# Performance work log

Measured on AMD Instinct MI355X. Metric: run time of the kernel, lower is better.

## Reference

```python
import jax, jax.numpy as jnp
import numpy as np

N = 50000       # nodes
E = 800000      # edges (avg degree 16)
F_IN = 128      # in_feats
H = 128         # h_feats
C = 16          # num_classes
EPS = 1e-5      # BatchNorm eps


def setup_inputs() -> dict:
    key = jax.random.key(0)
    ks = jax.random.split(key, 26)
    rn = lambda k, shape: jax.random.normal(k, shape, dtype=jnp.float32) * 0.05
    zeros = lambda d: jnp.zeros((d,), jnp.float32)
    ones = lambda d: jnp.ones((d,), jnp.float32)
    return {
        "features": jax.random.normal(ks[0], (N, F_IN), dtype=jnp.float32),
        "src": jax.random.randint(ks[1], (E,), 0, N),
        "dst": jax.random.randint(ks[2], (E,), 0, N),
        # input_encoder
        "W_in": rn(ks[3], (F_IN, H)), "b_in": zeros(H),
        # SAGEConv layer 0: H -> 2H (fc_self, fc_neigh, bias)
        "Ws0": rn(ks[4], (H, 2 * H)), "Wn0": rn(ks[5], (H, 2 * H)), "bs0": zeros(2 * H),
        # BatchNorm1d(2H) eval-mode stats
        "g0": ones(2 * H), "bt0": zeros(2 * H),
        "m0": rn(ks[6], (2 * H,)),
        "v0": jax.random.uniform(ks[7], (2 * H,), jnp.float32, 0.5, 1.5),
        # SAGEConv layer 1: 2H -> H
        "Ws1": rn(ks[8], (2 * H, H)), "Wn1": rn(ks[9], (2 * H, H)), "bs1": zeros(H),
        # BatchNorm1d(H)
        "g1": ones(H), "bt1": zeros(H),
        "m1": rn(ks[10], (H,)),
        "v1": jax.random.uniform(ks[11], (H,), jnp.float32, 0.5, 1.5),
        # relation_encoder: 2H -> H
        "Wr": rn(ks[12], (2 * H, H)), "br": zeros(H),
        # classifier: H -> H//2 -> C
        "Wc1": rn(ks[13], (H, H // 2)), "bc1": zeros(H // 2),
        "Wc2": rn(ks[14], (H // 2, C)), "bc2": zeros(C),
    }


def _bn(x, g, b, m, v):
    # eval-mode BatchNorm1d with running stats
    return (x - m) * jax.lax.rsqrt(v + EPS) * g + b


def _sage(h, src, dst, Ws, Wn, b, inv_deg):
    # DGL SAGEConv 'mean': out = fc_self(h_dst) + fc_neigh(mean_{u in N(v)} h_u) + bias
    neigh = jax.ops.segment_sum(h[src], dst, num_segments=N) * inv_deg  # [N, d_in]
    return h @ Ws + neigh @ Wn + b


def reference(features, src, dst, W_in, b_in, Ws0, Wn0, bs0, g0, bt0, m0, v0,
              Ws1, Wn1, bs1, g1, bt1, m1, v1, Wr, br, Wc1, bc1, Wc2, bc2):
    deg = jax.ops.segment_sum(jnp.ones((E,), jnp.float32), dst, num_segments=N)
    inv_deg = (1.0 / jnp.maximum(deg, 1.0))[:, None]  # [N, 1]

    h0 = jax.nn.relu(features @ W_in + b_in)                       # [N, H]
    h = jax.nn.relu(_bn(_sage(h0, src, dst, Ws0, Wn0, bs0, inv_deg), g0, bt0, m0, v0))  # [N, 2H]
    h = jax.nn.relu(_bn(_sage(h, src, dst, Ws1, Wn1, bs1, inv_deg), g1, bt1, m1, v1))   # [N, H]

    h_final = jax.nn.relu(jnp.concatenate([h0, h], axis=1) @ Wr + br)  # [N, H]
    return jax.nn.relu(h_final @ Wc1 + bc1) @ Wc2 + bc2                # [N, C]
```

## Files before the change

kernel.cpp:

```cpp
#include <hip/hip_runtime.h>

typedef short v8s __attribute__((ext_vector_type(8)));
typedef float v4f __attribute__((ext_vector_type(4)));
typedef unsigned short u16;
typedef unsigned int u32;

#define NNODES 50000
#define NEDGES 800000
#define CSTRIDE 64

#define NB 512
#define BSPAN 98
#define BCAP 2048
#define EBLK 98
#define NBU 511

__device__ __forceinline__ float bf2f(u16 b) {
    u32 u = ((u32)b) << 16;
    return __builtin_bit_cast(float, u);
}
__device__ __forceinline__ u16 f2bf(float f) {
    u32 u = __builtin_bit_cast(u32, f);
    u32 r = (u + 0x7fffu + ((u >> 16) & 1u)) >> 16;
    return (u16)r;
}

struct PackDesc { const float* B1; const float* B2; int K1, K2, N, csplit, start; u16* out; };
struct PackArgs { PackDesc d[6]; int total; };

__global__ __launch_bounds__(256) void pack_all(PackArgs pa) {
    int tid = blockIdx.x * 256 + threadIdx.x;
    if (tid >= pa.total) return;
    int s = 0;
    for (int i = 1; i < 6; i++)
        if (tid >= pa.d[i].start) s = i;
    const PackDesc& D = pa.d[s];
    int t = tid - D.start;
    int frag = t >> 9;
    int rem = t & 511;
    int lane = rem >> 3;
    int j = rem & 7;
    int nf = D.N >> 4;
    int kt = frag / nf, nt = frag - kt * nf;
    int k = kt * 32 + (lane >> 4) * 8 + j;
    int n = nt * 16 + (lane & 15);
    float v;
    if (D.csplit)
        v = (n < D.csplit) ? D.B1[(size_t)k * D.csplit + n]
                           : D.B2[(size_t)k * (D.N - D.csplit) + (n - D.csplit)];
    else
        v = (k < D.K1) ? D.B1[(size_t)k * D.N + n]
                       : D.B2[(size_t)(k - D.K1) * D.N + n];
    D.out[t] = f2bf(v);
}

__global__ __launch_bounds__(256) void prep_epi(
    const float* b_in, const float* bs0, const float* g0, const float* bt0,
    const float* m0, const float* v0,
    const float* bs1, const float* g1, const float* bt1, const float* m1, const float* v1,
    const float* br, const float* bc1, const float* bc2,
    float* sc_in, float* sh_in, float* sc0, float* sh0, float* sc1, float* sh1,
    float* sc_r, float* sh_r, float* sh_c1, float* sh_c2) {
    int t = threadIdx.x;
    if (t < 128) { sc_in[t] = 1.f; sh_in[t] = b_in[t]; }
    if (t < 256) {
        float s = g0[t] * rsqrtf(v0[t] + 1e-5f);
        sc0[t] = s;
        sh0[t] = (bs0[t] - m0[t]) * s + bt0[t];
    }
    if (t < 128) {
        float s = g1[t] * rsqrtf(v1[t] + 1e-5f);
        sc1[t] = s;
        sh1[t] = (bs1[t] - m1[t]) * s + bt1[t];
    }
    if (t < 128) { sc_r[t] = 1.f; sh_r[t] = br[t]; }
    if (t < 64)  { sh_c1[t] = bc1[t]; }
    if (t < 16)  { sh_c2[t] = bc2[t]; }
}

template <int BN, int CW, int KT, int KSPLIT, bool RELU, bool F32OUT, bool AF32>
__device__ __forceinline__ void gemm_body(
    int bx,
    const void* __restrict__ A0v, int lda0,
    const void* __restrict__ A1v, int lda1,
    int M,
    const v8s* __restrict__ Bp,
    const float* __restrict__ scale, const float* __restrict__ shift,
    u16* __restrict__ C, float* __restrict__ Cf, int ldc) {
    constexpr int NFW = BN / 16 / CW;
    constexpr int RW = 4 / CW;
    int lane = threadIdx.x & 63;
    int wave = threadIdx.x >> 6;
    int colw = wave % CW;
    int roww = wave / CW;
    int quad = lane >> 4;
    int l16 = lane & 15;
    int base = bx * (64 * RW) + roww * 64;

    v4f acc[4][NFW];
#pragma unroll
    for (int rg = 0; rg < 4; rg++)
#pragma unroll
        for (int nt = 0; nt < NFW; nt++) acc[rg][nt] = (v4f)0.0f;

    size_t o0[4], o1[4];
#pragma unroll
    for (int rg = 0; rg < 4; rg++) {
        int r = base + rg * 16 + l16;
        if (r > M - 1) r = M - 1;
        o0[rg] = (size_t)r * lda0 + quad * 8;
        o1[rg] = (size_t)r * lda1 + quad * 8;
    }

    auto load_a = [&](const void* Av, size_t off) -> v8s {
        if constexpr (AF32) {
            const float* p = (const float*)Av + off;
            float4 x = *(const float4*)p;
            float4 y = *(const float4*)(p + 4);
            v8s a;
            a[0] = (short)f2bf(x.x); a[1] = (short)f2bf(x.y);
            a[2] = (short)f2bf(x.z); a[3] = (short)f2bf(x.w);
            a[4] = (short)f2bf(y.x); a[5] = (short)f2bf(y.y);
            a[6] = (short)f2bf(y.z); a[7] = (short)f2bf(y.w);
            return a;
        } else {
            return *(const v8s*)((const u16*)Av + off);
        }
    };

#pragma unroll
    for (int kt = 0; kt < KT; kt++) {
        v8s a[4];
#pragma unroll
        for (int rg = 0; rg < 4; rg++) {
            if (kt < KSPLIT) a[rg] = load_a(A0v, o0[rg] + kt * 32);
            else             a[rg] = load_a(A1v, o1[rg] + (size_t)(kt - KSPLIT) * 32);
        }
        const v8s* bb = Bp + (size_t)kt * (BN / 16) * 64 + (colw * NFW) * 64 + lane;
#pragma unroll
        for (int nt = 0; nt < NFW; nt++) {
            v8s b = bb[nt * 64];
#pragma unroll
            for (int rg = 0; rg < 4; rg++)
                acc[rg][nt] = __builtin_amdgcn_mfma_f32_16x16x32_bf16(a[rg], b, acc[rg][nt], 0, 0, 0);
        }
    }

    int colbase = colw * (NFW * 16);
#pragma unroll
    for (int rg = 0; rg < 4; rg++) {
        int rbase = base + rg * 16 + quad * 4;
#pragma unroll
        for (int nt = 0; nt < NFW; nt++) {
            int col = colbase + nt * 16 + l16;
            float s = scale[col], sh = shift[col];
#pragma unroll
            for (int i = 0; i < 4; i++) {
                int row = rbase + i;
                if (row < M) {
                    float v = acc[rg][nt][i] * s + sh;
                    if (RELU) v = v > 0.f ? v : 0.f;
                    if (F32OUT) Cf[(size_t)row * ldc + col] = v;
                    else C[(size_t)row * ldc + col] = f2bf(v);
                }
            }
        }
    }
}

__global__ __launch_bounds__(256) void mega_binA_h0(
    const int* __restrict__ src, const int* __restrict__ dst,
    int* __restrict__ gcur, u32* __restrict__ gbuf,
    const float* __restrict__ features,
    const v8s* __restrict__ Winp,
    const float* __restrict__ sc_in, const float* __restrict__ sh_in,
    u16* __restrict__ hcat0) {
    int bx = blockIdx.x;
    if (bx < EBLK) {
        __shared__ int hist[NB];
        __shared__ int lbase[NB];
        int t = threadIdx.x;
        for (int i = t; i < NB; i += 256) hist[i] = 0;
        __syncthreads();
        int ebase = bx * 8192;
#pragma unroll
        for (int c = 0; c < 8; c++) {
            int e0 = ebase + c * 1024 + t * 4;
            if (e0 + 4 <= NEDGES) {
                int4 d4 = *(const int4*)(dst + e0);
                atomicAdd(&hist[d4.x / BSPAN], 1);
                atomicAdd(&hist[d4.y / BSPAN], 1);
                atomicAdd(&hist[d4.z / BSPAN], 1);
                atomicAdd(&hist[d4.w / BSPAN], 1);
            } else {
#pragma unroll
                for (int j = 0; j < 4; j++) {
                    int e = e0 + j;
                    if (e < NEDGES) atomicAdd(&hist[dst[e] / BSPAN], 1);
                }
            }
        }
        __syncthreads();
        for (int i = t; i < NB; i += 256) {
            int c = hist[i];
            lbase[i] = c ? atomicAdd(&gcur[i], c) : 0;
            hist[i] = 0;
        }
        __syncthreads();
#pragma unroll
        for (int c = 0; c < 8; c++) {
            int e0 = ebase + c * 1024 + t * 4;
            if (e0 + 4 <= NEDGES) {
                int4 s4 = *(const int4*)(src + e0);
                int4 d4 = *(const int4*)(dst + e0);
                int ss[4] = {s4.x, s4.y, s4.z, s4.w};
                int dd[4] = {d4.x, d4.y, d4.z, d4.w};
#pragma unroll
                for (int j = 0; j < 4; j++) {
                    int b = dd[j] / BSPAN;
                    int dl = dd[j] - b * BSPAN;
                    int p = atomicAdd(&hist[b], 1);
                    int idx = lbase[b] + p;
                    if (idx < BCAP)
                        gbuf[(size_t)b * BCAP + idx] = ((u32)dl << 16) | (u32)ss[j];
                }
            } else {
#pragma unroll
                for (int j = 0; j < 4; j++) {
                    int e = e0 + j;
                    if (e < NEDGES) {
                        int d = dst[e];
                        int b = d / BSPAN;
                        int dl = d - b * BSPAN;
                        int p = atomicAdd(&hist[b], 1);
                        int idx = lbase[b] + p;
                        if (idx < BCAP)
                            gbuf[(size_t)b * BCAP + idx] = ((u32)dl << 16) | (u32)src[e];
                    }
                }
            }
        }
    } else {
        gemm_body<128, 4, 4, 4, true, false, true>(
            bx - EBLK, features, 128, features, 128, NNODES,
            Winp, sc_in, sh_in, hcat0, nullptr, 256);
    }
}

__global__ __launch_bounds__(1024) void fill_bg(
    const u32* __restrict__ gbuf, const int* __restrict__ gcur,
    u16* __restrict__ csr, int* __restrict__ cursor,
    const u16* __restrict__ H, u16* __restrict__ D) {
    __shared__ u16 lcsr[BSPAN * CSTRIDE];
    __shared__ int lcur[BSPAN];
    int b = blockIdx.x;
    int t = threadIdx.x;
    int v0 = b * BSPAN;
    int span = NNODES - v0;
    if (span > BSPAN) span = BSPAN;
    for (int i = t; i < BSPAN; i += 1024) lcur[i] = 0;
    __syncthreads();
    int cnt = gcur[b];
    if (cnt > BCAP) cnt = BCAP;
    for (int i = t; i < cnt; i += 1024) {
        u32 pk = gbuf[(size_t)b * BCAP + i];
        int dl = pk >> 16;
        int p = atomicAdd(&lcur[dl], 1);
        if (p < CSTRIDE) lcsr[(dl << 6) + p] = (u16)(pk & 0xffffu);
    }
    __syncthreads();
    {
        const u32* lw = (const u32*)lcsr;
        u32* gw = (u32*)(csr + ((size_t)v0 << 6));
        int nw = span * (CSTRIDE / 2);
        for (int i = t; i < nw; i += 1024) gw[i] = lw[i];
        for (int i = t; i < span; i += 1024) cursor[v0 + i] = lcur[i];
    }
    int lane = t & 63;
    int wv = t >> 6;
    for (int i = wv; i < span; i += 16) {
        int d = lcur[i];
        if (d > CSTRIDE) d = CSTRIDE;
        float s = 1.0f / (float)(d > 0 ? d : 1);
        const u16* Hl = H + lane * 2;
        const u16* nl = &lcsr[i << 6];
        float a0 = 0.f, a1 = 0.f, b0 = 0.f, b1 = 0.f;
        float c0 = 0.f, c1 = 0.f, d0 = 0.f, d1 = 0.f;
        int e = 0;
        for (; e + 4 <= d; e += 4) {
            int u0 = nl[e], u1 = nl[e + 1], u2 = nl[e + 2], u3 = nl[e + 3];
            u32 w0 = *(const u32*)(Hl + (size_t)u0 * 256);
            u32 w1 = *(const u32*)(Hl + (size_t)u1 * 256);
            u32 w2 = *(const u32*)(Hl + (size_t)u2 * 256);
            u32 w3 = *(const u32*)(Hl + (size_t)u3 * 256);
            a0 += bf2f((u16)w0); a1 += bf2f((u16)(w0 >> 16));
            b0 += bf2f((u16)w1); b1 += bf2f((u16)(w1 >> 16));
            c0 += bf2f((u16)w2); c1 += bf2f((u16)(w2 >> 16));
            d0 += bf2f((u16)w3); d1 += bf2f((u16)(w3 >> 16));
        }
        for (; e < d; e++) {
            int u = nl[e];
            u32 w = *(const u32*)(Hl + (size_t)u * 256);
            a0 += bf2f((u16)w); a1 += bf2f((u16)(w >> 16));
        }
        a0 = (a0 + b0) + (c0 + d0);
        a1 = (a1 + b1) + (c1 + d1);
        u32 o = (u32)f2bf(a0 * s) | ((u32)f2bf(a1 * s) << 16);
        *(u32*)(D + (size_t)(v0 + i) * 256 + lane * 2) = o;
    }
}

__global__ __launch_bounds__(256) void gemm_h1ps(
    const u16* __restrict__ A,
    const v8s* __restrict__ B0,
    const float* __restrict__ sc0, const float* __restrict__ sh0,
    const v8s* __restrict__ B1,
    u16* __restrict__ ps, int M) {
    constexpr int LSTR = 264;
    __shared__ u16 h1s[64 * LSTR];
    int lane = threadIdx.x & 63;
    int wave = threadIdx.x >> 6;
    int quad = lane >> 4;
    int l16 = lane & 15;
    int base = blockIdx.x * 64;

    v4f acc[4][4];
#pragma unroll
    for (int rg = 0; rg < 4; rg++)
#pragma unroll
        for (int nt = 0; nt < 4; nt++) acc[rg][nt] = (v4f)0.0f;

    size_t o0[4];
#pragma unroll
    for (int rg = 0; rg < 4; rg++) {
        int r = base + rg * 16 + l16;
        if (r > M - 1) r = M - 1;
        o0[rg] = (size_t)r * 256 + quad * 8;
    }

#pragma unroll
    for (int kt = 0; kt < 8; kt++) {
        v8s a[4];
#pragma unroll
        for (int rg = 0; rg < 4; rg++) a[rg] = *(const v8s*)(A + o0[rg] + kt * 32);
        const v8s* bb = B0 + (size_t)kt * 16 * 64 + (wave * 4) * 64 + lane;
#pragma unroll
        for (int nt = 0; nt < 4; nt++) {
            v8s b = bb[nt * 64];
#pragma unroll
            for (int rg = 0; rg < 4; rg++)
                acc[rg][nt] = __builtin_amdgcn_mfma_f32_16x16x32_bf16(a[rg], b, acc[rg][nt], 0, 0, 0);
        }
    }
    int colbase = wave * 64;
#pragma unroll
    for (int rg = 0; rg < 4; rg++) {
        int rowL = rg * 16 + quad * 4;
#pragma unroll
        for (int nt = 0; nt < 4; nt++) {
            int col = colbase + nt * 16 + l16;
            float s = sc0[col], sh = sh0[col];
#pragma unroll
            for (int i = 0; i < 4; i++) {
                float v = acc[rg][nt][i] * s + sh;
                v = v > 0.f ? v : 0.f;
                h1s[(rowL + i) * LSTR + col] = f2bf(v);
            }
        }
    }
    __syncthreads();

#pragma unroll
    for (int rg = 0; rg < 4; rg++)
#pragma unroll
        for (int nt = 0; nt < 4; nt++) acc[rg][nt] = (v4f)0.0f;
#pragma unroll
    for (int kt = 0; kt < 8; kt++) {
        v8s a[4];
#pragma unroll
        for (int rg = 0; rg < 4; rg++)
            a[rg] = *(const v8s*)(&h1s[(rg * 16 + l16) * LSTR + quad * 8 + kt * 32]);
        const v8s* bb = B1 + (size_t)kt * 16 * 64 + (wave * 4) * 64 + lane;
#pragma unroll
        for (int nt = 0; nt < 4; nt++) {
            v8s b = bb[nt * 64];
#pragma unroll
            for (int rg = 0; rg < 4; rg++)
                acc[rg][nt] = __builtin_amdgcn_mfma_f32_16x16x32_bf16(a[rg], b, acc[rg][nt], 0, 0, 0);
        }
    }
#pragma unroll
    for (int rg = 0; rg < 4; rg++) {
        int rbase = base + rg * 16 + quad * 4;
#pragma unroll
        for (int nt = 0; nt < 4; nt++) {
            int col = colbase + nt * 16 + l16;
#pragma unroll
            for (int i = 0; i < 4; i++) {
                int row = rbase + i;
                if (row < M) ps[(size_t)row * 256 + col] = f2bf(acc[rg][nt][i]);
            }
        }
    }
}

__global__ __launch_bounds__(256) void agg_h2(
    const int* __restrict__ cursor, const u16* __restrict__ csr,
    const u16* __restrict__ ps,
    const float* __restrict__ sc1, const float* __restrict__ sh1,
    u16* __restrict__ h2, int n) {
    int v = blockIdx.x * 4 + (threadIdx.x >> 6);
    if (v >= n) return;
    int lane = threadIdx.x & 63;
    int d = cursor[v];
    if (d > CSTRIDE) d = CSTRIDE;
    int e0 = v << 6;
    int e1 = e0 + d;
    float s = 1.0f / (float)(d > 0 ? d : 1);
    const u16* Pn = ps + 128 + lane * 2;
    float a0 = 0.f, a1 = 0.f, b0 = 0.f, b1 = 0.f;
    float c0 = 0.f, c1 = 0.f, d0 = 0.f, d1 = 0.f;
    int e = e0;
    for (; e + 4 <= e1; e += 4) {
        int u0 = csr[e], u1 = csr[e + 1], u2 = csr[e + 2], u3 = csr[e + 3];
        u32 w0 = *(const u32*)(Pn + (size_t)u0 * 256);
        u32 w1 = *(const u32*)(Pn + (size_t)u1 * 256);
        u32 w2 = *(const u32*)(Pn + (size_t)u2 * 256);
        u32 w3 = *(const u32*)(Pn + (size_t)u3 * 256);
        a0 += bf2f((u16)w0); a1 += bf2f((u16)(w0 >> 16));
        b0 += bf2f((u16)w1); b1 += bf2f((u16)(w1 >> 16));
        c0 += bf2f((u16)w2); c1 += bf2f((u16)(w2 >> 16));
        d0 += bf2f((u16)w3); d1 += bf2f((u16)(w3 >> 16));
    }
    for (; e < e1; e++) {
        int u = csr[e];
        u32 w = *(const u32*)(Pn + (size_t)u * 256);
        a0 += bf2f((u16)w); a1 += bf2f((u16)(w >> 16));
    }
    a0 = (a0 + b0) + (c0 + d0);
    a1 = (a1 + b1) + (c1 + d1);
    u32 wv = *(const u32*)(ps + (size_t)v * 256 + lane * 2);
    int col = lane * 2;
    float x0 = (bf2f((u16)wv) + a0 * s) * sc1[col] + sh1[col];
    float x1 = (bf2f((u16)(wv >> 16)) + a1 * s) * sc1[col + 1] + sh1[col + 1];
    x0 = x0 > 0.f ? x0 : 0.f;
    x1 = x1 > 0.f ? x1 : 0.f;
    u32 o = (u32)f2bf(x0) | ((u32)f2bf(x1) << 16);
    *(u32*)(h2 + (size_t)v * 128 + lane * 2) = o;
}

__global__ __launch_bounds__(256) void gemm_chain(
    const u16* __restrict__ hcat0,
    const u16* __restrict__ h2,
    const v8s* __restrict__ Wrp, const float* __restrict__ sc_r, const float* __restrict__ sh_r,
    const v8s* __restrict__ Wm1p, const float* __restrict__ sh_c1,
    const v8s* __restrict__ Wm2p, const float* __restrict__ sh_c2,
    float* __restrict__ out, int M) {
    constexpr int LS = 136;
    __shared__ u16 tile[64 * LS];
    int lane = threadIdx.x & 63;
    int wv = threadIdx.x >> 6;
    int quad = lane >> 4;
    int l16 = lane & 15;
    int base = blockIdx.x * 64;

    v4f acc[4][2];
#pragma unroll
    for (int rg = 0; rg < 4; rg++)
#pragma unroll
        for (int nt = 0; nt < 2; nt++) acc[rg][nt] = (v4f)0.0f;
    size_t o0[4], o1[4];
#pragma unroll
    for (int rg = 0; rg < 4; rg++) {
        int r = base + rg * 16 + l16;
        if (r > M - 1) r = M - 1;
        o0[rg] = (size_t)r * 256 + quad * 8;
        o1[rg] = (size_t)r * 128 + quad * 8;
    }
#pragma unroll
    for (int kt = 0; kt < 8; kt++) {
        v8s a[4];
#pragma unroll
        for (int rg = 0; rg < 4; rg++) {
            if (kt < 4) a[rg] = *(const v8s*)(hcat0 + o0[rg] + kt * 32);
            else        a[rg] = *(const v8s*)(h2 + o1[rg] + (size_t)(kt - 4) * 32);
        }
        const v8s* bb = Wrp + (size_t)kt * 8 * 64 + (wv * 2) * 64 + lane;
#pragma unroll
        for (int nt = 0; nt < 2; nt++) {
            v8s b = bb[nt * 64];
#pragma unroll
            for (int rg = 0; rg < 4; rg++)
                acc[rg][nt] = __builtin_amdgcn_mfma_f32_16x16x32_bf16(a[rg], b, acc[rg][nt], 0, 0, 0);
        }
    }
    {
        int colbase = wv * 32;
#pragma unroll
        for (int rg = 0; rg < 4; rg++) {
            int rowL = rg * 16 + quad * 4;
#pragma unroll
            for (int nt = 0; nt < 2; nt++) {
                int col = colbase + nt * 16 + l16;
                float s = sc_r[col], sh = sh_r[col];
#pragma unroll
                for (int i = 0; i < 4; i++) {
                    float v = acc[rg][nt][i] * s + sh;
                    v = v > 0.f ? v : 0.f;
                    tile[(rowL + i) * LS + col] = f2bf(v);
                }
            }
        }
    }
    __syncthreads();

    v4f a2[4];
#pragma unroll
    for (int rg = 0; rg < 4; rg++) a2[rg] = (v4f)0.0f;
#pragma unroll
    for (int kt = 0; kt < 4; kt++) {
        v8s a[4];
#pragma unroll
        for (int rg = 0; rg < 4; rg++)
            a[rg] = *(const v8s*)(&tile[(rg * 16 + l16) * LS + quad * 8 + kt * 32]);
        v8s b = Wm1p[(size_t)kt * 4 * 64 + wv * 64 + lane];
#pragma unroll
        for (int rg = 0; rg < 4; rg++)
            a2[rg] = __builtin_amdgcn_mfma_f32_16x16x32_bf16(a[rg], b, a2[rg], 0, 0, 0);
    }
    __syncthreads();
    {
        int col = wv * 16 + l16;
        float sh = sh_c1[col];
#pragma unroll
        for (int rg = 0; rg < 4; rg++) {
            int rowL = rg * 16 + quad * 4;
#pragma unroll
            for (int i = 0; i < 4; i++) {
                float v = a2[rg][i] + sh;
                v = v > 0.f ? v : 0.f;
                tile[(rowL + i) * LS + col] = f2bf(v);
            }
        }
    }
    __syncthreads();

    v4f a3 = (v4f)0.0f;
#pragma unroll
    for (int kt = 0; kt < 2; kt++) {
        v8s a = *(const v8s*)(&tile[(wv * 16 + l16) * LS + quad * 8 + kt * 32]);
        v8s b = Wm2p[kt * 64 + lane];
        a3 = __builtin_amdgcn_mfma_f32_16x16x32_bf16(a, b, a3, 0, 0, 0);
    }
    int row = base + wv * 16 + quad * 4;
    float sh = sh_c2[l16];
#pragma unroll
    for (int i = 0; i < 4; i++) {
        int r = row + i;
        if (r < M) out[(size_t)r * 16 + l16] = a3[i] + sh;
    }
}

extern "C" void kernel_launch(void* const* d_in, const int* in_sizes, int n_in,
                              void* d_out, int out_size, void* d_ws, size_t ws_size,
                              hipStream_t stream) {
    const int N = NNODES;
    const float* features = (const float*)d_in[0];
    const int* src = (const int*)d_in[1];
    const int* dst = (const int*)d_in[2];
    float* out = (float*)d_out;

    char* w = (char*)d_ws;
    auto alloc = [&](size_t bytes) -> char* {
        char* p = w;
        w += (bytes + 255) & ~(size_t)255;
        return p;
    };
    int*   cursor = (int*)alloc((size_t)N * 4);
    u16*   csr    = (u16*)alloc((size_t)N * CSTRIDE * 2);
    u16*   hcat0  = (u16*)alloc((size_t)N * 256 * 2);
    u16*   ps     = (u16*)alloc((size_t)N * 256 * 2);
    u16*   h2     = (u16*)alloc((size_t)N * 128 * 2);
    u32*   gbuf   = (u32*)alloc((size_t)NB * BCAP * 4);
    int*   gcur   = (int*)alloc((size_t)NB * 4);
    u16*   Winp   = (u16*)alloc(128 * 128 * 2);
    u16*   Wc0p   = (u16*)alloc(256 * 256 * 2);
    u16*   Wsn1p  = (u16*)alloc(256 * 256 * 2);
    u16*   Wrp    = (u16*)alloc(256 * 128 * 2);
    u16*   Wm1p   = (u16*)alloc(128 * 64 * 2);
    u16*   Wm2p   = (u16*)alloc(64 * 16 * 2);
    float* sc_in = (float*)alloc(128 * 4); float* sh_in = (float*)alloc(128 * 4);
    float* sc0   = (float*)alloc(256 * 4); float* sh0   = (float*)alloc(256 * 4);
    float* sc1   = (float*)alloc(128 * 4); float* sh1   = (float*)alloc(128 * 4);
    float* sc_r  = (float*)alloc(128 * 4); float* sh_r  = (float*)alloc(128 * 4);
    float* sh_c1 = (float*)alloc(64 * 4);
    float* sh_c2 = (float*)alloc(16 * 4);

    hipMemsetAsync(gcur, 0, (size_t)NB * 4, stream);
    prep_epi<<<1, 256, 0, stream>>>((const float*)d_in[4], (const float*)d_in[7],
                                    (const float*)d_in[8], (const float*)d_in[9],
                                    (const float*)d_in[10], (const float*)d_in[11],
                                    (const float*)d_in[14], (const float*)d_in[15],
                                    (const float*)d_in[16], (const float*)d_in[17],
                                    (const float*)d_in[18], (const float*)d_in[20],
                                    (const float*)d_in[22], (const float*)d_in[24],
                                    sc_in, sh_in, sc0, sh0, sc1, sh1,
                                    sc_r, sh_r, sh_c1, sh_c2);

    PackArgs pa;
    int st = 0;
    auto seg = [&](int i, const float* B1, const float* B2, int K1, int K2,
                   int Nn, int csp, u16* o) {
        pa.d[i] = {B1, B2, K1, K2, Nn, csp, st, o};
        st += (K1 + K2) * Nn;
    };
    seg(0, (const float*)d_in[3], nullptr, 128, 0, 128, 0, Winp);
    seg(1, (const float*)d_in[5], (const float*)d_in[6], 128, 128, 256, 0, Wc0p);
    seg(2, (const float*)d_in[12], (const float*)d_in[13], 256, 0, 256, 128, Wsn1p);
    seg(3, (const float*)d_in[19], nullptr, 256, 0, 128, 0, Wrp);
    seg(4, (const float*)d_in[21], nullptr, 128, 0, 64, 0, Wm1p);
    seg(5, (const float*)d_in[23], nullptr, 64, 0, 16, 0, Wm2p);
    pa.total = st;
    pack_all<<<(st + 255) / 256, 256, 0, stream>>>(pa);

    int gb64 = (N + 63) / 64;
    mega_binA_h0<<<EBLK + gb64, 256, 0, stream>>>(
        src, dst, gcur, gbuf, features, (const v8s*)Winp, sc_in, sh_in, hcat0);
    fill_bg<<<NBU, 1024, 0, stream>>>(gbuf, gcur, csr, cursor, hcat0, hcat0 + 128);
    gemm_h1ps<<<gb64, 256, 0, stream>>>(hcat0, (const v8s*)Wc0p, sc0, sh0,
                                        (const v8s*)Wsn1p, ps, N);
    agg_h2<<<(N + 3) / 4, 256, 0, stream>>>(cursor, csr, ps, sc1, sh1, h2, N);
    gemm_chain<<<gb64, 256, 0, stream>>>(
        hcat0, h2, (const v8s*)Wrp, sc_r, sh_r,
        (const v8s*)Wm1p, sh_c1, (const v8s*)Wm2p, sh_c2, out, N);
}
```

Before: 265.0 us.

## Fuse neighbor-mean gathers into the consuming GEMM kernels via shared memory

The layer-0 neighbor mean moves out of the CSR fill kernel and into the h1/ps GEMM kernel, which gathers each 64-row tile's neighbor means into LDS and feeds them to the MFMA loop. The layer-1 aggregation kernel is folded into the final chain GEMM the same way, so the hcat0 upper half and the h2 intermediate are never written to or re-read from global memory, and one launch disappears. The gather loop is unrolled by 8 for more memory-level parallelism, and h0 now has a compact 128-wide stride. In exchange, GEMM blocks stall on latency-bound gathers before their MFMA work, and the added LDS per block may reduce occupancy.

```diff
diff --git a/kernel.cpp b/kernel.cpp
--- a/kernel.cpp
+++ b/kernel.cpp
@@ -174,7 +174,7 @@
     const float* __restrict__ features,
     const v8s* __restrict__ Winp,
     const float* __restrict__ sc_in, const float* __restrict__ sh_in,
-    u16* __restrict__ hcat0) {
+    u16* __restrict__ h0) {
     int bx = blockIdx.x;
     if (bx < EBLK) {
         __shared__ int hist[NB];
@@ -243,14 +243,13 @@
     } else {
         gemm_body<128, 4, 4, 4, true, false, true>(
             bx - EBLK, features, 128, features, 128, NNODES,
-            Winp, sc_in, sh_in, hcat0, nullptr, 256);
-    }
-}
-
-__global__ __launch_bounds__(1024) void fill_bg(
+            Winp, sc_in, sh_in, h0, nullptr, 128);
+    }
+}
+
+__global__ __launch_bounds__(256) void fill_b(
     const u32* __restrict__ gbuf, const int* __restrict__ gcur,
-    u16* __restrict__ csr, int* __restrict__ cursor,
-    const u16* __restrict__ H, u16* __restrict__ D) {
+    u16* __restrict__ csr, int* __restrict__ cursor) {
     __shared__ u16 lcsr[BSPAN * CSTRIDE];
     __shared__ int lcur[BSPAN];
     int b = blockIdx.x;
@@ -258,65 +257,83 @@
     int v0 = b * BSPAN;
     int span = NNODES - v0;
     if (span > BSPAN) span = BSPAN;
-    for (int i = t; i < BSPAN; i += 1024) lcur[i] = 0;
+    for (int i = t; i < BSPAN; i += 256) lcur[i] = 0;
     __syncthreads();
     int cnt = gcur[b];
     if (cnt > BCAP) cnt = BCAP;
-    for (int i = t; i < cnt; i += 1024) {
+    for (int i = t; i < cnt; i += 256) {
         u32 pk = gbuf[(size_t)b * BCAP + i];
         int dl = pk >> 16;
         int p = atomicAdd(&lcur[dl], 1);
         if (p < CSTRIDE) lcsr[(dl << 6) + p] = (u16)(pk & 0xffffu);
     }
     __syncthreads();
-    {
-        const u32* lw = (const u32*)lcsr;
-        u32* gw = (u32*)(csr + ((size_t)v0 << 6));
-        int nw = span * (CSTRIDE / 2);
-        for (int i = t; i < nw; i += 1024) gw[i] = lw[i];
-        for (int i = t; i < span; i += 1024) cursor[v0 + i] = lcur[i];
-    }
-    int lane = t & 63;
-    int wv = t >> 6;
-    for (int i = wv; i < span; i += 16) {
-        int d = lcur[i];
-        if (d > CSTRIDE) d = CSTRIDE;
-        float s = 1.0f / (float)(d > 0 ? d : 1);
-        const u16* Hl = H + lane * 2;
-        const u16* nl = &lcsr[i << 6];
-        float a0 = 0.f, a1 = 0.f, b0 = 0.f, b1 = 0.f;
-        float c0 = 0.f, c1 = 0.f, d0 = 0.f, d1 = 0.f;
-        int e = 0;
-        for (; e + 4 <= d; e += 4) {
-            int u0 = nl[e], u1 = nl[e + 1], u2 = nl[e + 2], u3 = nl[e + 3];
-            u32 w0 = *(const u32*)(Hl + (size_t)u0 * 256);
-            u32 w1 = *(const u32*)(Hl + (size_t)u1 * 256);
-            u32 w2 = *(const u32*)(Hl + (size_t)u2 * 256);
-            u32 w3 = *(const u32*)(Hl + (size_t)u3 * 256);
-            a0 += bf2f((u16)w0); a1 += bf2f((u16)(w0 >> 16));
-            b0 += bf2f((u16)w1); b1 += bf2f((u16)(w1 >> 16));
-            c0 += bf2f((u16)w2); c1 += bf2f((u16)(w2 >> 16));
-            d0 += bf2f((u16)w3); d1 += bf2f((u16)(w3 >> 16));
-        }
-        for (; e < d; e++) {
-            int u = nl[e];
-            u32 w = *(const u32*)(Hl + (size_t)u * 256);
-            a0 += bf2f((u16)w); a1 += bf2f((u16)(w >> 16));
-        }
-        a0 = (a0 + b0) + (c0 + d0);
-        a1 = (a1 + b1) + (c1 + d1);
-        u32 o = (u32)f2bf(a0 * s) | ((u32)f2bf(a1 * s) << 16);
-        *(u32*)(D + (size_t)(v0 + i) * 256 + lane * 2) = o;
-    }
-}
-
-__global__ __launch_bounds__(256) void gemm_h1ps(
-    const u16* __restrict__ A,
+    const u32* lw = (const u32*)lcsr;
+    u32* gw = (u32*)(csr + ((size_t)v0 << 6));
+    int nw = span * (CSTRIDE / 2);
+    for (int i = t; i < nw; i += 256) gw[i] = lw[i];
+    for (int i = t; i < span; i += 256) cursor[v0 + i] = lcur[i];
+}
+
+__device__ __forceinline__ u32 gather_mean2(
+    const u16* __restrict__ nl, int d, const u16* __restrict__ Hl, int ldh) {
+    float a0 = 0.f, a1 = 0.f, b0 = 0.f, b1 = 0.f;
+    float c0 = 0.f, c1 = 0.f, d0 = 0.f, d1 = 0.f;
+    float e0 = 0.f, e1 = 0.f, f0 = 0.f, f1 = 0.f;
+    float g0 = 0.f, g1 = 0.f, h0_ = 0.f, h1_ = 0.f;
+    int e = 0;
+    for (; e + 8 <= d; e += 8) {
+        int u0 = nl[e], u1 = nl[e + 1], u2 = nl[e + 2], u3 = nl[e + 3];
+        int u4 = nl[e + 4], u5 = nl[e + 5], u6 = nl[e + 6], u7 = nl[e + 7];
+        u32 w0 = *(const u32*)(Hl + (size_t)u0 * ldh);
+        u32 w1 = *(const u32*)(Hl + (size_t)u1 * ldh);
+        u32 w2 = *(const u32*)(Hl + (size_t)u2 * ldh);
+        u32 w3 = *(const u32*)(Hl + (size_t)u3 * ldh);
+        u32 w4 = *(const u32*)(Hl + (size_t)u4 * ldh);
+        u32 w5 = *(const u32*)(Hl + (size_t)u5 * ldh);
+        u32 w6 = *(const u32*)(Hl + (size_t)u6 * ldh);
+        u32 w7 = *(const u32*)(Hl + (size_t)u7 * ldh);
+        a0 += bf2f((u16)w0); a1 += bf2f((u16)(w0 >> 16));
+        b0 += bf2f((u16)w1); b1 += bf2f((u16)(w1 >> 16));
+        c0 += bf2f((u16)w2); c1 += bf2f((u16)(w2 >> 16));
+        d0 += bf2f((u16)w3); d1 += bf2f((u16)(w3 >> 16));
+        e0 += bf2f((u16)w4); e1 += bf2f((u16)(w4 >> 16));
+        f0 += bf2f((u16)w5); f1 += bf2f((u16)(w5 >> 16));
+        g0 += bf2f((u16)w6); g1 += bf2f((u16)(w6 >> 16));
+        h0_ += bf2f((u16)w7); h1_ += bf2f((u16)(w7 >> 16));
+    }
+    for (; e + 4 <= d; e += 4) {
+        int u0 = nl[e], u1 = nl[e + 1], u2 = nl[e + 2], u3 = nl[e + 3];
+        u32 w0 = *(const u32*)(Hl + (size_t)u0 * ldh);
+        u32 w1 = *(const u32*)(Hl + (size_t)u1 * ldh);
+        u32 w2 = *(const u32*)(Hl + (size_t)u2 * ldh);
+        u32 w3 = *(const u32*)(Hl + (size_t)u3 * ldh);
+        a0 += bf2f((u16)w0); a1 += bf2f((u16)(w0 >> 16));
+        b0 += bf2f((u16)w1); b1 += bf2f((u16)(w1 >> 16));
+        c0 += bf2f((u16)w2); c1 += bf2f((u16)(w2 >> 16));
+        d0 += bf2f((u16)w3); d1 += bf2f((u16)(w3 >> 16));
+    }
+    for (; e < d; e++) {
+        int u = nl[e];
+        u32 w = *(const u32*)(Hl + (size_t)u * ldh);
+        a0 += bf2f((u16)w); a1 += bf2f((u16)(w >> 16));
+    }
+    float s = 1.0f / (float)(d > 0 ? d : 1);
+    float r0 = ((a0 + b0) + (c0 + d0)) + ((e0 + f0) + (g0 + h0_));
+    float r1 = ((a1 + b1) + (c1 + d1)) + ((e1 + f1) + (g1 + h1_));
+    return (u32)f2bf(r0 * s) | ((u32)f2bf(r1 * s) << 16);
+}
+
+__global__ __launch_bounds__(256) void h1ps_g(
+    const int* __restrict__ cursor, const u16* __restrict__ csr,
+    const u16* __restrict__ h0,
     const v8s* __restrict__ B0,
     const float* __restrict__ sc0, const float* __restrict__ sh0,
     const v8s* __restrict__ B1,
     u16* __restrict__ ps, int M) {
+    constexpr int NLS = 136;
     constexpr int LSTR = 264;
+    __shared__ u16 n0s[64 * NLS];
     __shared__ u16 h1s[64 * LSTR];
     int lane = threadIdx.x & 63;
     int wave = threadIdx.x >> 6;
@@ -324,6 +341,18 @@
     int l16 = lane & 15;
     int base = blockIdx.x * 64;
 
+    for (int i = wave; i < 64; i += 4) {
+        int v = base + i;
+        u32 o = 0;
+        if (v < M) {
+            int d = cursor[v];
+            if (d > CSTRIDE) d = CSTRIDE;
+            o = gather_mean2(csr + ((size_t)v << 6), d, h0 + lane * 2, 128);
+        }
+        *(u32*)(&n0s[i * NLS + lane * 2]) = o;
+    }
+    __syncthreads();
+
     v4f acc[4][4];
 #pragma unroll
     for (int rg = 0; rg < 4; rg++)
@@ -335,14 +364,17 @@
     for (int rg = 0; rg < 4; rg++) {
         int r = base + rg * 16 + l16;
         if (r > M - 1) r = M - 1;
-        o0[rg] = (size_t)r * 256 + quad * 8;
+        o0[rg] = (size_t)r * 128 + quad * 8;
     }
 
 #pragma unroll
     for (int kt = 0; kt < 8; kt++) {
         v8s a[4];
 #pragma unroll
-        for (int rg = 0; rg < 4; rg++) a[rg] = *(const v8s*)(A + o0[rg] + kt * 32);
+        for (int rg = 0; rg < 4; rg++) {
+            if (kt < 4) a[rg] = *(const v8s*)(h0 + o0[rg] + kt * 32);
+            else        a[rg] = *(const v8s*)(&n0s[(rg * 16 + l16) * NLS + quad * 8 + (kt - 4) * 32]);
+        }
         const v8s* bb = B0 + (size_t)kt * 16 * 64 + (wave * 4) * 64 + lane;
 #pragma unroll
         for (int nt = 0; nt < 4; nt++) {
@@ -404,59 +436,17 @@
     }
 }
 
-__global__ __launch_bounds__(256) void agg_h2(
+__global__ __launch_bounds__(256) void chain_all(
     const int* __restrict__ cursor, const u16* __restrict__ csr,
     const u16* __restrict__ ps,
     const float* __restrict__ sc1, const float* __restrict__ sh1,
-    u16* __restrict__ h2, int n) {
-    int v = blockIdx.x * 4 + (threadIdx.x >> 6);
-    if (v >= n) return;
-    int lane = threadIdx.x & 63;
-    int d = cursor[v];
-    if (d > CSTRIDE) d = CSTRIDE;
-    int e0 = v << 6;
-    int e1 = e0 + d;
-    float s = 1.0f / (float)(d > 0 ? d : 1);
-    const u16* Pn = ps + 128 + lane * 2;
-    float a0 = 0.f, a1 = 0.f, b0 = 0.f, b1 = 0.f;
-    float c0 = 0.f, c1 = 0.f, d0 = 0.f, d1 = 0.f;
-    int e = e0;
-    for (; e + 4 <= e1; e += 4) {
-        int u0 = csr[e], u1 = csr[e + 1], u2 = csr[e + 2], u3 = csr[e + 3];
-        u32 w0 = *(const u32*)(Pn + (size_t)u0 * 256);
-        u32 w1 = *(const u32*)(Pn + (size_t)u1 * 256);
-        u32 w2 = *(const u32*)(Pn + (size_t)u2 * 256);
-        u32 w3 = *(const u32*)(Pn + (size_t)u3 * 256);
-        a0 += bf2f((u16)w0); a1 += bf2f((u16)(w0 >> 16));
-        b0 += bf2f((u16)w1); b1 += bf2f((u16)(w1 >> 16));
-        c0 += bf2f((u16)w2); c1 += bf2f((u16)(w2 >> 16));
-        d0 += bf2f((u16)w3); d1 += bf2f((u16)(w3 >> 16));
-    }
-    for (; e < e1; e++) {
-        int u = csr[e];
-        u32 w = *(const u32*)(Pn + (size_t)u * 256);
-        a0 += bf2f((u16)w); a1 += bf2f((u16)(w >> 16));
-    }
-    a0 = (a0 + b0) + (c0 + d0);
-    a1 = (a1 + b1) + (c1 + d1);
-    u32 wv = *(const u32*)(ps + (size_t)v * 256 + lane * 2);
-    int col = lane * 2;
-    float x0 = (bf2f((u16)wv) + a0 * s) * sc1[col] + sh1[col];
-    float x1 = (bf2f((u16)(wv >> 16)) + a1 * s) * sc1[col + 1] + sh1[col + 1];
-    x0 = x0 > 0.f ? x0 : 0.f;
-    x1 = x1 > 0.f ? x1 : 0.f;
-    u32 o = (u32)f2bf(x0) | ((u32)f2bf(x1) << 16);
-    *(u32*)(h2 + (size_t)v * 128 + lane * 2) = o;
-}
-
-__global__ __launch_bounds__(256) void gemm_chain(
-    const u16* __restrict__ hcat0,
-    const u16* __restrict__ h2,
+    const u16* __restrict__ h0,
     const v8s* __restrict__ Wrp, const float* __restrict__ sc_r, const float* __restrict__ sh_r,
     const v8s* __restrict__ Wm1p, const float* __restrict__ sh_c1,
     const v8s* __restrict__ Wm2p, const float* __restrict__ sh_c2,
     float* __restrict__ out, int M) {
     constexpr int LS = 136;
+    __shared__ u16 h2s[64 * LS];
     __shared__ u16 tile[64 * LS];
     int lane = threadIdx.x & 63;
     int wv = threadIdx.x >> 6;
@@ -464,26 +454,44 @@
     int l16 = lane & 15;
     int base = blockIdx.x * 64;
 
+    for (int i = wv; i < 64; i += 4) {
+        int v = base + i;
+        u32 o = 0;
+        if (v < M) {
+            int d = cursor[v];
+            if (d > CSTRIDE) d = CSTRIDE;
+            u32 nm = gather_mean2(csr + ((size_t)v << 6), d, ps + 128 + lane * 2, 256);
+            u32 sv = *(const u32*)(ps + (size_t)v * 256 + lane * 2);
+            int col = lane * 2;
+            float x0 = (bf2f((u16)sv) + bf2f((u16)nm)) * sc1[col] + sh1[col];
+            float x1 = (bf2f((u16)(sv >> 16)) + bf2f((u16)(nm >> 16))) * sc1[col + 1] + sh1[col + 1];
+            x0 = x0 > 0.f ? x0 : 0.f;
+            x1 = x1 > 0.f ? x1 : 0.f;
+            o = (u32)f2bf(x0) | ((u32)f2bf(x1) << 16);
+        }
+        *(u32*)(&h2s[i * LS + lane * 2]) = o;
+    }
+    __syncthreads();
+
     v4f acc[4][2];
 #pragma unroll
     for (int rg = 0; rg < 4; rg++)
 #pragma unroll
         for (int nt = 0; nt < 2; nt++) acc[rg][nt] = (v4f)0.0f;
-    size_t o0[4], o1[4];
+    size_t o0[4];
 #pragma unroll
     for (int rg = 0; rg < 4; rg++) {
         int r = base + rg * 16 + l16;
         if (r > M - 1) r = M - 1;
-        o0[rg] = (size_t)r * 256 + quad * 8;
-        o1[rg] = (size_t)r * 128 + quad * 8;
+        o0[rg] = (size_t)r * 128 + quad * 8;
     }
 #pragma unroll
     for (int kt = 0; kt < 8; kt++) {
         v8s a[4];
 #pragma unroll
         for (int rg = 0; rg < 4; rg++) {
-            if (kt < 4) a[rg] = *(const v8s*)(hcat0 + o0[rg] + kt * 32);
-            else        a[rg] = *(const v8s*)(h2 + o1[rg] + (size_t)(kt - 4) * 32);
+            if (kt < 4) a[rg] = *(const v8s*)(h0 + o0[rg] + kt * 32);
+            else        a[rg] = *(const v8s*)(&h2s[(rg * 16 + l16) * LS + quad * 8 + (kt - 4) * 32]);
         }
         const v8s* bb = Wrp + (size_t)kt * 8 * 64 + (wv * 2) * 64 + lane;
 #pragma unroll
@@ -578,9 +586,8 @@
     };
     int*   cursor = (int*)alloc((size_t)N * 4);
     u16*   csr    = (u16*)alloc((size_t)N * CSTRIDE * 2);
-    u16*   hcat0  = (u16*)alloc((size_t)N * 256 * 2);
+    u16*   h0     = (u16*)alloc((size_t)N * 128 * 2);
     u16*   ps     = (u16*)alloc((size_t)N * 256 * 2);
-    u16*   h2     = (u16*)alloc((size_t)N * 128 * 2);
     u32*   gbuf   = (u32*)alloc((size_t)NB * BCAP * 4);
     int*   gcur   = (int*)alloc((size_t)NB * 4);
     u16*   Winp   = (u16*)alloc(128 * 128 * 2);
@@ -625,12 +632,12 @@
 
     int gb64 = (N + 63) / 64;
     mega_binA_h0<<<EBLK + gb64, 256, 0, stream>>>(
-        src, dst, gcur, gbuf, features, (const v8s*)Winp, sc_in, sh_in, hcat0);
-    fill_bg<<<NBU, 1024, 0, stream>>>(gbuf, gcur, csr, cursor, hcat0, hcat0 + 128);
-    gemm_h1ps<<<gb64, 256, 0, stream>>>(hcat0, (const v8s*)Wc0p, sc0, sh0,
-                                        (const v8s*)Wsn1p, ps, N);
-    agg_h2<<<(N + 3) / 4, 256, 0, stream>>>(cursor, csr, ps, sc1, sh1, h2, N);
-    gemm_chain<<<gb64, 256, 0, stream>>>(
-        hcat0, h2, (const v8s*)Wrp, sc_r, sh_r,
+        src, dst, gcur, gbuf, features, (const v8s*)Winp, sc_in, sh_in, h0);
+    fill_b<<<NBU, 256, 0, stream>>>(gbuf, gcur, csr, cursor);
+    h1ps_g<<<gb64, 256, 0, stream>>>(cursor, csr, h0, (const v8s*)Wc0p, sc0, sh0,
+                                     (const v8s*)Wsn1p, ps, N);
+    chain_all<<<gb64, 256, 0, stream>>>(
+        cursor, csr, ps, sc1, sh1, h0,
+        (const v8s*)Wrp, sc_r, sh_r,
         (const v8s*)Wm1p, sh_c1, (const v8s*)Wm2p, sh_c2, out, N);
 }
```

Result: slower. 339.5 us (+28.1%).
